# Kernel optimization log

Measured on AMD Instinct MI355X. Metric: run time of the kernel, lower is better.

## Reference

```python
import jax, jax.numpy as jnp
import numpy as np

B, T, C, H = 4, 2048, 1024, 16
D = C // H  # head_dim = 64

def setup_inputs() -> dict:
    key = jax.random.key(0)
    k1, k2, k3 = jax.random.split(key, 3)
    x = jax.random.normal(k1, (B, T, C), dtype=jnp.float32)
    w_qkv = jax.random.normal(k2, (C, 3 * C), dtype=jnp.float32) * (C ** -0.5)
    w_proj = jax.random.normal(k3, (C, C), dtype=jnp.float32) * (C ** -0.5)
    b_proj = jnp.zeros((C,), dtype=jnp.float32)
    return {"x": x, "w_qkv": w_qkv, "w_proj": w_proj, "b_proj": b_proj}

def reference(x, w_qkv, w_proj, b_proj):
    Bx, Tx, Cx = x.shape
    qkv = x @ w_qkv  # [B,T,3C]
    q, k, v = jnp.split(qkv, 3, axis=-1)
    # [B,T,H,D] -> [B,H,T,D]
    q = q.reshape(Bx, Tx, H, D).transpose(0, 2, 1, 3)
    k = k.reshape(Bx, Tx, H, D).transpose(0, 2, 1, 3)
    v = v.reshape(Bx, Tx, H, D).transpose(0, 2, 1, 3)
    scale = 1.0 / np.sqrt(D).astype(np.float32)
    att = jnp.einsum('bhqd,bhkd->bhqk', q, k) * scale  # [B,H,T,T]
    causal = jnp.tril(jnp.ones((Tx, Tx), dtype=bool))
    att = jnp.where(causal, att, -jnp.inf)
    att = jax.nn.softmax(att, axis=-1)
    y = jnp.einsum('bhqk,bhkd->bhqd', att, v)  # [B,H,T,D]
    y = y.transpose(0, 2, 1, 3).reshape(Bx, Tx, Cx)
    return y @ w_proj + b_proj
```

## Files before the change

kernel.cpp:

```cpp
#include <hip/hip_runtime.h>

typedef unsigned short u16;
typedef unsigned int u32;
typedef __attribute__((ext_vector_type(8))) short bf16x8;
typedef __attribute__((ext_vector_type(4))) float f32x4;
typedef __attribute__((ext_vector_type(16))) float f32x16;
typedef __attribute__((ext_vector_type(4))) unsigned short u16x4;

#define MFMA16(a, b, c) __builtin_amdgcn_mfma_f32_16x16x32_bf16((a), (b), (c), 0, 0, 0)
#define MFMA32(a, b, c) __builtin_amdgcn_mfma_f32_32x32x16_bf16((a), (b), (c), 0, 0, 0)

__device__ __forceinline__ u16 f2bf(float f) {
  union { float f; unsigned int i; } v; v.f = f;
  return (u16)((v.i + 0x7FFFu + ((v.i >> 16) & 1u)) >> 16);
}
__device__ __forceinline__ float exp2a(float x) {
  float r; asm("v_exp_f32 %0, %1" : "=v"(r) : "v"(x)); return r;
}
__device__ __forceinline__ u32 cvtpk(float lo, float hi) {
  u32 d; asm("v_cvt_pk_bf16_f32 %0, %1, %2" : "=v"(d) : "v"(lo), "v"(hi)); return d;
}
__device__ __forceinline__ void gl2lds16(const u16* g, u16* l) {
  __builtin_amdgcn_global_load_lds(
      (const __attribute__((address_space(1))) void*)g,
      (__attribute__((address_space(3))) void*)l, 16, 0, 0);
}

__global__ __launch_bounds__(256) void k_ingest(const float* __restrict__ src,
                                                u16* __restrict__ dst, int n8) {
  const int i = blockIdx.x * 256 + threadIdx.x;
  if (i >= n8) return;
  const float* s = src + (size_t)i * 8;
  float4 a = *(const float4*)(s);
  float4 b = *(const float4*)(s + 4);
  union { u16 o[8]; int4 v; } u;
  u.o[0] = f2bf(a.x); u.o[1] = f2bf(a.y); u.o[2] = f2bf(a.z); u.o[3] = f2bf(a.w);
  u.o[4] = f2bf(b.x); u.o[5] = f2bf(b.y); u.o[6] = f2bf(b.z); u.o[7] = f2bf(b.w);
  *(int4*)(&dst[(size_t)i * 8]) = u.v;
}

__global__ __launch_bounds__(256) void k_transpose(const float* __restrict__ src,
                                                   u16* __restrict__ dst, int R, int C) {
  __shared__ u16 tile[64][65];
  const int c0 = blockIdx.x * 64, r0 = blockIdx.y * 64;
  const int t = threadIdx.x;
#pragma unroll
  for (int i = 0; i < 16; ++i) {
    int e = i * 256 + t, rr = e >> 6, cc = e & 63;
    tile[rr][cc] = f2bf(src[(size_t)(r0 + rr) * C + c0 + cc]);
  }
  __syncthreads();
#pragma unroll
  for (int i = 0; i < 16; ++i) {
    int e = i * 256 + t, rr = e >> 6, cc = e & 63;
    dst[(size_t)(c0 + rr) * R + r0 + cc] = tile[cc][rr];
  }
}

template <int QKV>
__global__ __launch_bounds__(256) void k_gemm(
    const u16* __restrict__ A, const u16* __restrict__ Bt,
    const float* __restrict__ bias, float* __restrict__ Cf,
    u16* __restrict__ Qb, u16* __restrict__ Kb, u16* __restrict__ VTb,
    int M, int N, int K) {
  __shared__ __attribute__((aligned(16))) u16 As[128 * 32];
  __shared__ __attribute__((aligned(16))) u16 Bs[128 * 32];
  const int bn = blockIdx.x, bm = blockIdx.y;
  const int t = threadIdx.x, lane = t & 63, w = t >> 6;
  const int wr = w >> 1, wc = w & 1;
  const int rh = lane & 15, kg = lane >> 4;
  const int srow = lane >> 2, sk8 = (lane & 3) << 3;

  f32x4 acc[4][4];
#pragma unroll
  for (int mi = 0; mi < 4; ++mi)
#pragma unroll
    for (int ni = 0; ni < 4; ++ni) acc[mi][ni] = (f32x4)0.0f;

  for (int k0 = 0; k0 < K; k0 += 32) {
#pragma unroll
    for (int i = 0; i < 2; ++i) {
      const int r0 = w * 32 + i * 16;
      gl2lds16(&A[(size_t)(bm * 128 + r0 + srow) * K + k0 + sk8], &As[r0 * 32]);
      gl2lds16(&Bt[(size_t)(bn * 128 + r0 + srow) * K + k0 + sk8], &Bs[r0 * 32]);
    }
    asm volatile("s_waitcnt vmcnt(0)" ::: "memory");
    __syncthreads();

    bf16x8 af[4], bfr[4];
#pragma unroll
    for (int mi = 0; mi < 4; ++mi)
      af[mi] = *(const bf16x8*)(&As[(wr * 64 + mi * 16 + rh) * 32 + kg * 8]);
#pragma unroll
    for (int ni = 0; ni < 4; ++ni)
      bfr[ni] = *(const bf16x8*)(&Bs[(wc * 64 + ni * 16 + rh) * 32 + kg * 8]);
    __builtin_amdgcn_s_setprio(1);
#pragma unroll
    for (int mi = 0; mi < 4; ++mi)
#pragma unroll
      for (int ni = 0; ni < 4; ++ni)
        acc[mi][ni] = MFMA16(af[mi], bfr[ni], acc[mi][ni]);
    __builtin_amdgcn_s_setprio(0);
    __syncthreads();
  }

  if (QKV == 0) {
    const int rbase = bm * 128 + wr * 64;
    const int cbase = bn * 128 + wc * 64;
#pragma unroll
    for (int ni = 0; ni < 4; ++ni) {
      const int col = cbase + ni * 16 + rh;
      const float bv = bias ? bias[col] : 0.0f;
#pragma unroll
      for (int mi = 0; mi < 4; ++mi) {
#pragma unroll
        for (int r = 0; r < 4; ++r) {
          int row = rbase + mi * 16 + kg * 4 + r;
          Cf[(size_t)row * N + col] = acc[mi][ni][r] + bv;
        }
      }
    }
  } else {
    const float SCQ = 0.125f * 1.44269504f;
    const int rowbase = bm * 128 + wr * 64;
    const int b = rowbase >> 11;
    const int tb = rowbase & 2047;
    const int cbase = bn * 128 + wc * 64;
    const int role = cbase >> 10;
    const int h = (cbase & 1023) >> 6;
    const int bh = b * 16 + h;
#pragma unroll
    for (int ni = 0; ni < 4; ++ni) {
      const int d = ni * 16 + rh;
#pragma unroll
      for (int mi = 0; mi < 4; ++mi) {
        const int tt = tb + mi * 16 + kg * 4;
        if (role == 2) {
          u16x4 pk;
#pragma unroll
          for (int r = 0; r < 4; ++r) pk[r] = f2bf(acc[mi][ni][r]);
          *(u16x4*)(&VTb[((size_t)bh * 64 + d) * 2048 + tt]) = pk;
        } else {
          u16* dst = (role == 0) ? Qb : Kb;
          const float sc = (role == 0) ? SCQ : 1.0f;
#pragma unroll
          for (int r = 0; r < 4; ++r)
            dst[((size_t)bh * 2048 + tt + r) * 64 + d] = f2bf(acc[mi][ni][r] * sc);
        }
      }
    }
  }
}

__global__ __launch_bounds__(64, 2) void k_attn(const u16* __restrict__ Qb,
                                                const u16* __restrict__ Kb,
                                                const u16* __restrict__ VTb,
                                                u16* __restrict__ Y) {
  const int bh = blockIdx.x;
  const int sb = 31 - (int)blockIdx.y;
  const int lane = threadIdx.x & 63;
  const int q31 = lane & 31, hi = lane >> 5;
  const int qA = sb * 64 + q31;
  const int qBr = sb * 64 + 32 + q31;
  const u16* Qh = Qb + (size_t)bh * 2048 * 64;
  const u16* Kh = Kb + (size_t)bh * 2048 * 64;
  const u16* Vh = VTb + (size_t)bh * 64 * 2048;
  const int b = bh >> 4, h = bh & 15;

  bf16x8 qfA[4], qfB[4];
#pragma unroll
  for (int d = 0; d < 4; ++d) {
    qfA[d] = *(const bf16x8*)(&Qh[(size_t)qA * 64 + d * 16 + hi * 8]);
    qfB[d] = *(const bf16x8*)(&Qh[(size_t)qBr * 64 + d * 16 + hi * 8]);
  }

  f32x16 oA0 = (f32x16)0.0f, oA1 = (f32x16)0.0f;
  f32x16 oB0 = (f32x16)0.0f, oB1 = (f32x16)0.0f;
  float mA = -1e30f, sA = 0.0f, mB = -1e30f, sB = 0.0f;

  const int nt = 2 * sb + 2;
  for (int tt = 0; tt < nt; ++tt) {
    const int j0 = tt * 32;
    const bool aAct = tt < nt - 1;

    bf16x8 kf[4];
#pragma unroll
    for (int d = 0; d < 4; ++d)
      kf[d] = *(const bf16x8*)(&Kh[(size_t)(j0 + q31) * 64 + d * 16 + hi * 8]);
    const bf16x8 vf0 = *(const bf16x8*)(&Vh[(size_t)q31 * 2048 + j0 + hi * 8]);
    const bf16x8 vf1 = *(const bf16x8*)(&Vh[(size_t)q31 * 2048 + j0 + 16 + hi * 8]);
    const bf16x8 vf2 = *(const bf16x8*)(&Vh[(size_t)(32 + q31) * 2048 + j0 + hi * 8]);
    const bf16x8 vf3 = *(const bf16x8*)(&Vh[(size_t)(32 + q31) * 2048 + j0 + 16 + hi * 8]);

    f32x16 stB = (f32x16)0.0f;
    __builtin_amdgcn_s_setprio(1);
#pragma unroll
    for (int d = 0; d < 4; ++d) stB = MFMA32(kf[d], qfB[d], stB);
    f32x16 stA = (f32x16)0.0f;
    if (aAct) {
#pragma unroll
      for (int d = 0; d < 4; ++d) stA = MFMA32(kf[d], qfA[d], stA);
    }
    __builtin_amdgcn_s_setprio(0);

    if (tt == nt - 2) {
#pragma unroll
      for (int r = 0; r < 16; ++r) {
        const int kcol = (r & 3) + 8 * (r >> 2) + 4 * hi;
        if (kcol > q31) stA[r] = -1e30f;
      }
    }
    if (tt == nt - 1) {
#pragma unroll
      for (int r = 0; r < 16; ++r) {
        const int kcol = (r & 3) + 8 * (r >> 2) + 4 * hi;
        if (kcol > q31) stB[r] = -1e30f;
      }
    }

    union { u32 w4[4]; bf16x8 f; } paA0, paA1, paB0, paB1;
    if (aAct) {
      float mx = fmaxf(
          fmaxf(fmaxf(fmaxf(stA[0], stA[1]), fmaxf(stA[2], stA[3])),
                fmaxf(fmaxf(stA[4], stA[5]), fmaxf(stA[6], stA[7]))),
          fmaxf(fmaxf(fmaxf(stA[8], stA[9]), fmaxf(stA[10], stA[11])),
                fmaxf(fmaxf(stA[12], stA[13]), fmaxf(stA[14], stA[15]))));
      if (__any(mx - mA > 8.0f)) {
        mx = fmaxf(mx, __shfl_xor(mx, 32));
        const float mn = fmaxf(mA, mx);
        const float scf = exp2a(mA - mn);
        mA = mn; sA *= scf; oA0 *= scf; oA1 *= scf;
      }
      float p[16];
#pragma unroll
      for (int r = 0; r < 16; ++r) p[r] = exp2a(stA[r] - mA);
      sA += (((p[0] + p[1]) + (p[2] + p[3])) + ((p[4] + p[5]) + (p[6] + p[7]))) +
            (((p[8] + p[9]) + (p[10] + p[11])) + ((p[12] + p[13]) + (p[14] + p[15])));
      u32 D0 = cvtpk(p[0], p[1]),   D1 = cvtpk(p[2], p[3]);
      u32 D2 = cvtpk(p[4], p[5]),   D3 = cvtpk(p[6], p[7]);
      u32 D4 = cvtpk(p[8], p[9]),   D5 = cvtpk(p[10], p[11]);
      u32 D6 = cvtpk(p[12], p[13]), D7 = cvtpk(p[14], p[15]);
      u32 X0 = __shfl_xor(D0, 32), X1 = __shfl_xor(D1, 32);
      u32 X2 = __shfl_xor(D2, 32), X3 = __shfl_xor(D3, 32);
      u32 X4 = __shfl_xor(D4, 32), X5 = __shfl_xor(D5, 32);
      u32 X6 = __shfl_xor(D6, 32), X7 = __shfl_xor(D7, 32);
      paA0.w4[0] = hi ? X2 : D0; paA0.w4[1] = hi ? X3 : D1;
      paA0.w4[2] = hi ? D2 : X0; paA0.w4[3] = hi ? D3 : X1;
      paA1.w4[0] = hi ? X6 : D4; paA1.w4[1] = hi ? X7 : D5;
      paA1.w4[2] = hi ? D6 : X4; paA1.w4[3] = hi ? D7 : X5;
    }

    {
      float mx = fmaxf(
          fmaxf(fmaxf(fmaxf(stB[0], stB[1]), fmaxf(stB[2], stB[3])),
                fmaxf(fmaxf(stB[4], stB[5]), fmaxf(stB[6], stB[7]))),
          fmaxf(fmaxf(fmaxf(stB[8], stB[9]), fmaxf(stB[10], stB[11])),
                fmaxf(fmaxf(stB[12], stB[13]), fmaxf(stB[14], stB[15]))));
      if (__any(mx - mB > 8.0f)) {
        mx = fmaxf(mx, __shfl_xor(mx, 32));
        const float mn = fmaxf(mB, mx);
        const float scf = exp2a(mB - mn);
        mB = mn; sB *= scf; oB0 *= scf; oB1 *= scf;
      }
      float p[16];
#pragma unroll
      for (int r = 0; r < 16; ++r) p[r] = exp2a(stB[r] - mB);
      sB += (((p[0] + p[1]) + (p[2] + p[3])) + ((p[4] + p[5]) + (p[6] + p[7]))) +
            (((p[8] + p[9]) + (p[10] + p[11])) + ((p[12] + p[13]) + (p[14] + p[15])));
      u32 D0 = cvtpk(p[0], p[1]),   D1 = cvtpk(p[2], p[3]);
      u32 D2 = cvtpk(p[4], p[5]),   D3 = cvtpk(p[6], p[7]);
      u32 D4 = cvtpk(p[8], p[9]),   D5 = cvtpk(p[10], p[11]);
      u32 D6 = cvtpk(p[12], p[13]), D7 = cvtpk(p[14], p[15]);
      u32 X0 = __shfl_xor(D0, 32), X1 = __shfl_xor(D1, 32);
      u32 X2 = __shfl_xor(D2, 32), X3 = __shfl_xor(D3, 32);
      u32 X4 = __shfl_xor(D4, 32), X5 = __shfl_xor(D5, 32);
      u32 X6 = __shfl_xor(D6, 32), X7 = __shfl_xor(D7, 32);
      paB0.w4[0] = hi ? X2 : D0; paB0.w4[1] = hi ? X3 : D1;
      paB0.w4[2] = hi ? D2 : X0; paB0.w4[3] = hi ? D3 : X1;
      paB1.w4[0] = hi ? X6 : D4; paB1.w4[1] = hi ? X7 : D5;
      paB1.w4[2] = hi ? D6 : X4; paB1.w4[3] = hi ? D7 : X5;
    }

    __builtin_amdgcn_s_setprio(1);
    oB0 = MFMA32(vf0, paB0.f, oB0);
    oB0 = MFMA32(vf1, paB1.f, oB0);
    oB1 = MFMA32(vf2, paB0.f, oB1);
    oB1 = MFMA32(vf3, paB1.f, oB1);
    if (aAct) {
      oA0 = MFMA32(vf0, paA0.f, oA0);
      oA0 = MFMA32(vf1, paA1.f, oA0);
      oA1 = MFMA32(vf2, paA0.f, oA1);
      oA1 = MFMA32(vf3, paA1.f, oA1);
    }
    __builtin_amdgcn_s_setprio(0);
  }

  sA += __shfl_xor(sA, 32);
  sB += __shfl_xor(sB, 32);
  const float invA = 1.0f / sA, invB = 1.0f / sB;
  u16* yrowA = Y + ((size_t)b * 2048 + qA) * 1024 + h * 64;
  u16* yrowB = Y + ((size_t)b * 2048 + qBr) * 1024 + h * 64;
#pragma unroll
  for (int a = 0; a < 4; ++a) {
    u16x4 pk;
#pragma unroll
    for (int i = 0; i < 4; ++i) pk[i] = f2bf(oA0[a * 4 + i] * invA);
    *(u16x4*)(yrowA + a * 8 + 4 * hi) = pk;
#pragma unroll
    for (int i = 0; i < 4; ++i) pk[i] = f2bf(oA1[a * 4 + i] * invA);
    *(u16x4*)(yrowA + 32 + a * 8 + 4 * hi) = pk;
#pragma unroll
    for (int i = 0; i < 4; ++i) pk[i] = f2bf(oB0[a * 4 + i] * invB);
    *(u16x4*)(yrowB + a * 8 + 4 * hi) = pk;
#pragma unroll
    for (int i = 0; i < 4; ++i) pk[i] = f2bf(oB1[a * 4 + i] * invB);
    *(u16x4*)(yrowB + 32 + a * 8 + 4 * hi) = pk;
  }
}

extern "C" void kernel_launch(void* const* d_in, const int* in_sizes, int n_in,
                              void* d_out, int out_size, void* d_ws, size_t ws_size,
                              hipStream_t stream) {
  const float* x      = (const float*)d_in[0];
  const float* w_qkv  = (const float*)d_in[1];
  const float* w_proj = (const float*)d_in[2];
  const float* b_proj = (const float*)d_in[3];
  float* out = (float*)d_out;

  char* ws = (char*)d_ws;
  u16* wqkvT  = (u16*)(ws);
  u16* wprojT = (u16*)(ws + 6291456);
  u16* Qb     = (u16*)(ws + 8388608);
  u16* Kb     = (u16*)(ws + 25165824);
  u16* VTb    = (u16*)(ws + 41943040);
  u16* xb     = (u16*)(ws + 58720256);
  u16* Yb     = xb;

  k_ingest<<<4096, 256, 0, stream>>>(x, xb, 1048576);
  k_transpose<<<dim3(48, 16), 256, 0, stream>>>(w_qkv, wqkvT, 1024, 3072);
  k_transpose<<<dim3(16, 16), 256, 0, stream>>>(w_proj, wprojT, 1024, 1024);
  k_gemm<1><<<dim3(24, 64), 256, 0, stream>>>(xb, wqkvT, nullptr, nullptr,
                                              Qb, Kb, VTb, 8192, 3072, 1024);
  k_attn<<<dim3(64, 32), 64, 0, stream>>>(Qb, Kb, VTb, Yb);
  k_gemm<0><<<dim3(8, 64), 256, 0, stream>>>(Yb, wprojT, b_proj, out,
                                             nullptr, nullptr, nullptr, 8192, 1024, 1024);
}
```

Before: 213.4 us.

## Split long causal attention rows across two blocks and merge partials

The 16 longest query superblocks per head are split into two KV halves handled by separate blocks. Each half writes its running max, sum and unnormalized bf16 output to a scratch area placed in the output buffer, and a new combine kernel merges the two halves with log-sum-exp rescaling. This is meant to reduce load imbalance and tail effects from the causal triangle. It costs an extra kernel launch, partial-result traffic, and extra bf16 rounding of the unnormalized partial outputs.

```diff
diff --git a/kernel.cpp b/kernel.cpp
--- a/kernel.cpp
+++ b/kernel.cpp
@@ -13,6 +13,9 @@
 __device__ __forceinline__ u16 f2bf(float f) {
   union { float f; unsigned int i; } v; v.f = f;
   return (u16)((v.i + 0x7FFFu + ((v.i >> 16) & 1u)) >> 16);
+}
+__device__ __forceinline__ float b2f(u16 u) {
+  union { unsigned int i; float f; } v; v.i = ((unsigned int)u) << 16; return v.f;
 }
 __device__ __forceinline__ float exp2a(float x) {
   float r; asm("v_exp_f32 %0, %1" : "=v"(r) : "v"(x)); return r;
@@ -155,9 +158,26 @@
 __global__ __launch_bounds__(64, 2) void k_attn(const u16* __restrict__ Qb,
                                                 const u16* __restrict__ Kb,
                                                 const u16* __restrict__ VTb,
-                                                u16* __restrict__ Y) {
+                                                u16* __restrict__ Y,
+                                                char* __restrict__ part) {
   const int bh = blockIdx.x;
-  const int sb = 31 - (int)blockIdx.y;
+  const int y = (int)blockIdx.y;
+  int sb, t0, t1, half = 0;
+  bool spl;
+  if (y < 32) {
+    sb = 31 - (y >> 1);
+    half = y & 1;
+    const int hl = sb + 1;
+    t0 = half * hl;
+    t1 = t0 + hl;
+    spl = true;
+  } else {
+    sb = 47 - y;
+    t0 = 0;
+    t1 = 2 * sb + 2;
+    spl = false;
+  }
+  const int nt = 2 * sb + 2;
   const int lane = threadIdx.x & 63;
   const int q31 = lane & 31, hi = lane >> 5;
   const int qA = sb * 64 + q31;
@@ -178,8 +198,7 @@
   f32x16 oB0 = (f32x16)0.0f, oB1 = (f32x16)0.0f;
   float mA = -1e30f, sA = 0.0f, mB = -1e30f, sB = 0.0f;
 
-  const int nt = 2 * sb + 2;
-  for (int tt = 0; tt < nt; ++tt) {
+  for (int tt = t0; tt < t1; ++tt) {
     const int j0 = tt * 32;
     const bool aAct = tt < nt - 1;
 
@@ -297,25 +316,73 @@
 
   sA += __shfl_xor(sA, 32);
   sB += __shfl_xor(sB, 32);
-  const float invA = 1.0f / sA, invB = 1.0f / sB;
-  u16* yrowA = Y + ((size_t)b * 2048 + qA) * 1024 + h * 64;
-  u16* yrowB = Y + ((size_t)b * 2048 + qBr) * 1024 + h * 64;
-#pragma unroll
-  for (int a = 0; a < 4; ++a) {
-    u16x4 pk;
-#pragma unroll
-    for (int i = 0; i < 4; ++i) pk[i] = f2bf(oA0[a * 4 + i] * invA);
-    *(u16x4*)(yrowA + a * 8 + 4 * hi) = pk;
-#pragma unroll
-    for (int i = 0; i < 4; ++i) pk[i] = f2bf(oA1[a * 4 + i] * invA);
-    *(u16x4*)(yrowA + 32 + a * 8 + 4 * hi) = pk;
-#pragma unroll
-    for (int i = 0; i < 4; ++i) pk[i] = f2bf(oB0[a * 4 + i] * invB);
-    *(u16x4*)(yrowB + a * 8 + 4 * hi) = pk;
-#pragma unroll
-    for (int i = 0; i < 4; ++i) pk[i] = f2bf(oB1[a * 4 + i] * invB);
-    *(u16x4*)(yrowB + 32 + a * 8 + 4 * hi) = pk;
-  }
+
+  if (!spl) {
+    const float invA = 1.0f / sA, invB = 1.0f / sB;
+    u16* yrowA = Y + ((size_t)b * 2048 + qA) * 1024 + h * 64;
+    u16* yrowB = Y + ((size_t)b * 2048 + qBr) * 1024 + h * 64;
+#pragma unroll
+    for (int a = 0; a < 4; ++a) {
+      u16x4 pk;
+#pragma unroll
+      for (int i = 0; i < 4; ++i) pk[i] = f2bf(oA0[a * 4 + i] * invA);
+      *(u16x4*)(yrowA + a * 8 + 4 * hi) = pk;
+#pragma unroll
+      for (int i = 0; i < 4; ++i) pk[i] = f2bf(oA1[a * 4 + i] * invA);
+      *(u16x4*)(yrowA + 32 + a * 8 + 4 * hi) = pk;
+#pragma unroll
+      for (int i = 0; i < 4; ++i) pk[i] = f2bf(oB0[a * 4 + i] * invB);
+      *(u16x4*)(yrowB + a * 8 + 4 * hi) = pk;
+#pragma unroll
+      for (int i = 0; i < 4; ++i) pk[i] = f2bf(oB1[a * 4 + i] * invB);
+      *(u16x4*)(yrowB + 32 + a * 8 + 4 * hi) = pk;
+    }
+  } else {
+    const size_t pbase = ((size_t)(bh * 16 + (sb - 16)) * 2 + half) * 64;
+    char* pA = part + (pbase + q31) * 144;
+    char* pB = part + (pbase + 32 + q31) * 144;
+    if (!hi) {
+      ((float*)pA)[0] = mA; ((float*)pA)[1] = sA;
+      ((float*)pB)[0] = mB; ((float*)pB)[1] = sB;
+    }
+    u16* oA = (u16*)(pA + 8);
+    u16* oB = (u16*)(pB + 8);
+#pragma unroll
+    for (int a = 0; a < 4; ++a) {
+      u16x4 pk;
+#pragma unroll
+      for (int i = 0; i < 4; ++i) pk[i] = f2bf(oA0[a * 4 + i]);
+      *(u16x4*)(oA + a * 8 + 4 * hi) = pk;
+#pragma unroll
+      for (int i = 0; i < 4; ++i) pk[i] = f2bf(oA1[a * 4 + i]);
+      *(u16x4*)(oA + 32 + a * 8 + 4 * hi) = pk;
+#pragma unroll
+      for (int i = 0; i < 4; ++i) pk[i] = f2bf(oB0[a * 4 + i]);
+      *(u16x4*)(oB + a * 8 + 4 * hi) = pk;
+#pragma unroll
+      for (int i = 0; i < 4; ++i) pk[i] = f2bf(oB1[a * 4 + i]);
+      *(u16x4*)(oB + 32 + a * 8 + 4 * hi) = pk;
+    }
+  }
+}
+
+__global__ __launch_bounds__(256) void k_comb(const char* __restrict__ part,
+                                              u16* __restrict__ Y) {
+  const int g = blockIdx.x * 4 + (threadIdx.x >> 6);
+  const int d = threadIdx.x & 63;
+  const int bh = g >> 10, sbi = (g >> 6) & 15, r = g & 63;
+  const char* p1 = part + ((size_t)((bh * 16 + sbi) * 2 + 0) * 64 + r) * 144;
+  const char* p2 = part + ((size_t)((bh * 16 + sbi) * 2 + 1) * 64 + r) * 144;
+  const float m1 = ((const float*)p1)[0], s1 = ((const float*)p1)[1];
+  const float m2 = ((const float*)p2)[0], s2 = ((const float*)p2)[1];
+  const float mm = fmaxf(m1, m2);
+  const float e1 = exp2a(m1 - mm), e2 = exp2a(m2 - mm);
+  const float inv = 1.0f / (s1 * e1 + s2 * e2);
+  const float o1 = b2f(((const u16*)(p1 + 8))[d]);
+  const float o2 = b2f(((const u16*)(p2 + 8))[d]);
+  const int b = bh >> 4, h = bh & 15;
+  const int row = (16 + sbi) * 64 + r;
+  Y[((size_t)b * 2048 + row) * 1024 + h * 64 + d] = f2bf((o1 * e1 + o2 * e2) * inv);
 }
 
 extern "C" void kernel_launch(void* const* d_in, const int* in_sizes, int n_in,
@@ -335,13 +402,15 @@
   u16* VTb    = (u16*)(ws + 41943040);
   u16* xb     = (u16*)(ws + 58720256);
   u16* Yb     = xb;
+  char* part  = (char*)d_out;
 
   k_ingest<<<4096, 256, 0, stream>>>(x, xb, 1048576);
   k_transpose<<<dim3(48, 16), 256, 0, stream>>>(w_qkv, wqkvT, 1024, 3072);
   k_transpose<<<dim3(16, 16), 256, 0, stream>>>(w_proj, wprojT, 1024, 1024);
   k_gemm<1><<<dim3(24, 64), 256, 0, stream>>>(xb, wqkvT, nullptr, nullptr,
                                               Qb, Kb, VTb, 8192, 3072, 1024);
-  k_attn<<<dim3(64, 32), 64, 0, stream>>>(Qb, Kb, VTb, Yb);
+  k_attn<<<dim3(64, 48), 64, 0, stream>>>(Qb, Kb, VTb, Yb, part);
+  k_comb<<<16384, 256, 0, stream>>>(part, Yb);
   k_gemm<0><<<dim3(8, 64), 256, 0, stream>>>(Yb, wprojT, b_proj, out,
                                              nullptr, nullptr, nullptr, 8192, 1024, 1024);
 }
```

After: 220.7 us. +3.4%, slower.
